# Kernel optimization log

Measured on AMD Instinct MI355X. Metric: run time of the kernel, lower is better.

## Reference

```python
import jax, jax.numpy as jnp
import numpy as np

NUM_HEADS = 8
NUM_LAYER = 4


def setup_inputs() -> dict:
    key = jax.random.key(0)
    k1, k2, k3, k4, k5, k6, k7 = jax.random.split(key, 7)
    bs, num, C = 2, 2048, 256
    H0 = (jax.random.uniform(k1, (bs, num, num)) < 0.3).astype(jnp.float32)
    vertex_feat = jax.random.normal(k2, (bs, C, num), dtype=jnp.float32)
    edge_feat = jax.random.normal(k3, (bs, C, num), dtype=jnp.float32)
    s = 1.0 / np.sqrt(C)
    # Conv1d(kernel_size=1) weights, squeezed to [C_out, C_in]
    Wq = jax.random.uniform(k4, (C, C), minval=-s, maxval=s, dtype=jnp.float32)
    bq = jax.random.uniform(k5, (C,), minval=-s, maxval=s, dtype=jnp.float32)
    Wk = jax.random.uniform(k6, (C, C), minval=-s, maxval=s, dtype=jnp.float32)
    bk = jax.random.uniform(k7, (C,), minval=-s, maxval=s, dtype=jnp.float32)
    return {"H0": H0, "vertex_feat": vertex_feat, "edge_feat": edge_feat,
            "Wq": Wq, "bq": bq, "Wk": Wk, "bk": bk, "iter": 1}


def reference(H0, vertex_feat, edge_feat, Wq, bq, Wk, bk, iter):
    bs, num, _ = H0.shape
    C = vertex_feat.shape[1]
    h = NUM_HEADS
    d = C // h
    # 1x1 Conv1d == per-position linear; reshape to heads: [bs, h, d, num]
    Q = (jnp.einsum('oc,bcn->bon', Wq, vertex_feat) + bq[None, :, None]).reshape(bs, h, d, num)
    K = (jnp.einsum('oc,bcn->bon', Wk, edge_feat) + bk[None, :, None]).reshape(bs, h, d, num)
    attn = jnp.einsum('bhco,bhci->bhoi', Q, K) / np.sqrt(d)  # [bs, h, num, num]
    # attention_mask = (1 - H0).masked_fill((1-H0).bool(), -1e9)
    m = 1.0 - H0
    m = jnp.where(m != 0, jnp.float32(-1e9), m)
    score = jax.nn.sigmoid(attn + m[:, None, :, :]).sum(axis=1) / h  # [bs, num, num]
    # top-k row thresholding (k static: iter is a python int)
    k = max(1, round(num * 0.1 * (NUM_LAYER - 1 - iter)))
    topk_vals = jax.lax.top_k(score, k)[0]           # sorted descending
    a_min = topk_vals[..., -1:]                      # row-wise k-th largest
    W = jnp.where(score >= a_min, score, jnp.float32(0.0))
    H = jnp.where(W > 0, H0, jnp.float32(0.0))
    # degree normalizations (1e-10 keeps them finite; torch isinf branch is a no-op)
    De_n_1 = (1.0 / (H.sum(axis=1) + 1e-10))[..., None]  # [bs, num, 1]
    Dv_n_1 = (1.0 / (H.sum(axis=2) + 1e-10))[..., None]  # [bs, num, 1]
    # F.normalize(W.sum(dim=1), dim=1): L2 normalize with eps=1e-12
    W_edge = W.sum(axis=1)
    W_edge = W_edge / jnp.maximum(jnp.linalg.norm(W_edge, axis=1, keepdims=True), 1e-12)
    W_edge = W_edge[..., None]  # [bs, num, 1]
    return (H, W, De_n_1, Dv_n_1, W_edge)
```

## Files before the change

kernel.cpp:

```cpp
#include <hip/hip_runtime.h>
#include <math.h>

#define NUM 2048
#define CDIM 256
#define NUM_LAYER 4

typedef short bf16x8 __attribute__((ext_vector_type(8)));
typedef unsigned short u16x8 __attribute__((ext_vector_type(8)));
typedef float f32x4 __attribute__((ext_vector_type(4)));

static __device__ __forceinline__ unsigned short f2bf(float f) {
  unsigned u = __float_as_uint(f);
  unsigned r = 0x7FFFu + ((u >> 16) & 1u);
  return (unsigned short)((u + r) >> 16);
}
static __device__ __forceinline__ float bf2f(unsigned short h) {
  return __uint_as_float(((unsigned)h) << 16);
}

__global__ __launch_bounds__(256) void proj_kernel(
    const float* __restrict__ Wq, const float* __restrict__ bq,
    const float* __restrict__ Wk, const float* __restrict__ bk,
    const float* __restrict__ vf, const float* __restrict__ ef,
    unsigned short* __restrict__ Qhi, unsigned short* __restrict__ Qmd,
    unsigned short* __restrict__ Qlo, unsigned short* __restrict__ Khi,
    unsigned short* __restrict__ Kmd, unsigned short* __restrict__ Klo)
{
  const int z = blockIdx.z;
  const int b = z >> 1, mm2 = z & 1;
  const float* __restrict__ Wmat = mm2 ? Wk : Wq;
  const float* __restrict__ bias = mm2 ? bk : bq;
  const float* __restrict__ x = (mm2 ? ef : vf) + (size_t)b * CDIM * NUM;
  unsigned short* __restrict__ ohi = mm2 ? Khi : Qhi;
  unsigned short* __restrict__ omd = mm2 ? Kmd : Qmd;
  unsigned short* __restrict__ olo = mm2 ? Klo : Qlo;

  const int n0 = blockIdx.x * 64;
  const int o0 = blockIdx.y * 64;
  __shared__ float Xs[32][65];
  __shared__ float Ws[64][33];
  __shared__ float T[64][69];
  const int t = threadIdx.x;
  const int tx = t & 15, ty = t >> 4;

  float acc[4][4];
  #pragma unroll
  for (int a = 0; a < 4; a++)
    #pragma unroll
    for (int c = 0; c < 4; c++) acc[a][c] = 0.0f;

  for (int cc = 0; cc < CDIM; cc += 32) {
    #pragma unroll
    for (int e = 0; e < 2; e++) {
      int f = t * 2 + e;
      int row = f >> 4, c4 = f & 15;
      const float4 v = *(const float4*)(&x[(size_t)(cc + row) * NUM + n0 + c4 * 4]);
      Xs[row][c4*4+0] = v.x; Xs[row][c4*4+1] = v.y;
      Xs[row][c4*4+2] = v.z; Xs[row][c4*4+3] = v.w;
    }
    #pragma unroll
    for (int e = 0; e < 2; e++) {
      int f = t * 2 + e;
      int row = f >> 3, c4 = f & 7;
      const float4 v = *(const float4*)(&Wmat[(size_t)(o0 + row) * CDIM + cc + c4 * 4]);
      Ws[row][c4*4+0] = v.x; Ws[row][c4*4+1] = v.y;
      Ws[row][c4*4+2] = v.z; Ws[row][c4*4+3] = v.w;
    }
    __syncthreads();
    #pragma unroll
    for (int kk = 0; kk < 32; kk++) {
      float xv[4], wv[4];
      #pragma unroll
      for (int j = 0; j < 4; j++) xv[j] = Xs[kk][tx*4+j];
      #pragma unroll
      for (int j = 0; j < 4; j++) wv[j] = Ws[ty*4+j][kk];
      #pragma unroll
      for (int oi = 0; oi < 4; oi++)
        #pragma unroll
        for (int ni = 0; ni < 4; ni++)
          acc[oi][ni] = fmaf(wv[oi], xv[ni], acc[oi][ni]);
    }
    __syncthreads();
  }
  float bb[4];
  #pragma unroll
  for (int oi = 0; oi < 4; oi++) bb[oi] = bias[o0 + ty*4 + oi];
  #pragma unroll
  for (int ni = 0; ni < 4; ni++)
    #pragma unroll
    for (int oi = 0; oi < 4; oi++)
      T[tx*4+ni][ty*4+oi] = acc[oi][ni] + bb[oi];
  __syncthreads();
  const int n_l = t >> 2;
  const int oc  = (t & 3) * 16;
  float xv[16];
  #pragma unroll
  for (int j = 0; j < 16; j++) xv[j] = T[n_l][oc + j];
  unsigned short hi[16], md[16], lo[16];
  #pragma unroll
  for (int j = 0; j < 16; j++) {
    unsigned short h = f2bf(xv[j]);
    float r1 = xv[j] - bf2f(h);
    unsigned short mdj = f2bf(r1);
    float r2 = r1 - bf2f(mdj);
    hi[j] = h; md[j] = mdj; lo[j] = f2bf(r2);
  }
  const size_t gb = ((size_t)b * NUM + n0 + n_l) * CDIM + o0 + oc;
  *(u16x8*)&ohi[gb]   = *(u16x8*)&hi[0];
  *(u16x8*)&ohi[gb+8] = *(u16x8*)&hi[8];
  *(u16x8*)&omd[gb]   = *(u16x8*)&md[0];
  *(u16x8*)&omd[gb+8] = *(u16x8*)&md[8];
  *(u16x8*)&olo[gb]   = *(u16x8*)&lo[0];
  *(u16x8*)&olo[gb+8] = *(u16x8*)&lo[8];
}

__global__ __launch_bounds__(256) void score_kernel(
    const unsigned short* __restrict__ Qhi, const unsigned short* __restrict__ Qmd,
    const unsigned short* __restrict__ Qlo, const unsigned short* __restrict__ Khi,
    const unsigned short* __restrict__ Kmd, const unsigned short* __restrict__ Klo,
    const float* __restrict__ H0, float* __restrict__ score)
{
  const int b = blockIdx.z;
  const int i0 = blockIdx.x * 128;
  const int o0 = blockIdx.y * 128;
  const int t = threadIdx.x, lane = t & 63, wave = t >> 6;
  const int m = lane & 15, quad = lane >> 4;
  const int obl = (wave >> 1) * 64;
  const int ibl = (wave & 1) * 64;

  __shared__ unsigned short qsh[3][128][36];
  __shared__ unsigned short ksh[3][128][36];

  const int srow = t >> 2;
  const int schk = (t & 3) * 8;

  f32x4 ssum[4][4];
  #pragma unroll
  for (int a = 0; a < 4; a++)
    #pragma unroll
    for (int c = 0; c < 4; c++) ssum[a][c] = (f32x4){0.f, 0.f, 0.f, 0.f};

  const float SC = -1.4426950408889634f * 0.17677669529663687f;

  u16x8 pq[3][2], pk[3][2];
  #pragma unroll
  for (int e = 0; e < 2; e++) {
    const size_t go = ((size_t)b * NUM + o0 + srow + 64*e) * CDIM + schk;
    const size_t gi = ((size_t)b * NUM + i0 + srow + 64*e) * CDIM + schk;
    pq[0][e] = *(const u16x8*)&Qhi[go];
    pq[1][e] = *(const u16x8*)&Qmd[go];
    pq[2][e] = *(const u16x8*)&Qlo[go];
    pk[0][e] = *(const u16x8*)&Khi[gi];
    pk[1][e] = *(const u16x8*)&Kmd[gi];
    pk[2][e] = *(const u16x8*)&Klo[gi];
  }

  for (int h = 0; h < 8; h++) {
    __syncthreads();
    #pragma unroll
    for (int e = 0; e < 2; e++) {
      #pragma unroll
      for (int cp = 0; cp < 3; cp++) {
        *(u16x8*)&qsh[cp][srow + 64*e][schk] = pq[cp][e];
        *(u16x8*)&ksh[cp][srow + 64*e][schk] = pk[cp][e];
      }
    }
    __syncthreads();
    if (h < 7) {
      const int coff = (h + 1) * 32 + schk;
      #pragma unroll
      for (int e = 0; e < 2; e++) {
        const size_t go = ((size_t)b * NUM + o0 + srow + 64*e) * CDIM + coff;
        const size_t gi = ((size_t)b * NUM + i0 + srow + 64*e) * CDIM + coff;
        pq[0][e] = *(const u16x8*)&Qhi[go];
        pq[1][e] = *(const u16x8*)&Qmd[go];
        pq[2][e] = *(const u16x8*)&Qlo[go];
        pk[0][e] = *(const u16x8*)&Khi[gi];
        pk[1][e] = *(const u16x8*)&Kmd[gi];
        pk[2][e] = *(const u16x8*)&Klo[gi];
      }
    }
    bf16x8 a[4][3];
    #pragma unroll
    for (int ot = 0; ot < 4; ot++)
      #pragma unroll
      for (int cp = 0; cp < 3; cp++)
        a[ot][cp] = *(const bf16x8*)&qsh[cp][obl + ot*16 + m][quad*8];
    #pragma unroll
    for (int it = 0; it < 4; it++) {
      const bf16x8 b0 = *(const bf16x8*)&ksh[0][ibl + it*16 + m][quad*8];
      const bf16x8 b1 = *(const bf16x8*)&ksh[1][ibl + it*16 + m][quad*8];
      const bf16x8 b2 = *(const bf16x8*)&ksh[2][ibl + it*16 + m][quad*8];
      #pragma unroll
      for (int ot = 0; ot < 4; ot++) {
        f32x4 c = (f32x4){0.f, 0.f, 0.f, 0.f};
        c = __builtin_amdgcn_mfma_f32_16x16x32_bf16(a[ot][0], b0, c, 0, 0, 0);
        c = __builtin_amdgcn_mfma_f32_16x16x32_bf16(a[ot][0], b1, c, 0, 0, 0);
        c = __builtin_amdgcn_mfma_f32_16x16x32_bf16(a[ot][1], b0, c, 0, 0, 0);
        c = __builtin_amdgcn_mfma_f32_16x16x32_bf16(a[ot][1], b1, c, 0, 0, 0);
        c = __builtin_amdgcn_mfma_f32_16x16x32_bf16(a[ot][0], b2, c, 0, 0, 0);
        c = __builtin_amdgcn_mfma_f32_16x16x32_bf16(a[ot][2], b0, c, 0, 0, 0);
        #pragma unroll
        for (int r = 0; r < 4; r++)
          ssum[ot][it][r] += __builtin_amdgcn_rcpf(1.0f + __builtin_amdgcn_exp2f(c[r] * SC));
      }
    }
  }
  const int ob = o0 + obl, ib = i0 + ibl;
  #pragma unroll
  for (int ot = 0; ot < 4; ot++)
    #pragma unroll
    for (int it = 0; it < 4; it++)
      #pragma unroll
      for (int r = 0; r < 4; r++) {
        const int row = ob + ot*16 + quad*4 + r;
        const int col = ib + it*16 + m;
        const size_t idx = ((size_t)b * NUM + row) * NUM + col;
        score[idx] = H0[idx] * ssum[ot][it][r] * 0.125f;
      }
}

__global__ __launch_bounds__(256) void topk_apply_kernel(
    float* __restrict__ scoreW, float* __restrict__ Hout,
    const int* __restrict__ iterp, float* __restrict__ DvOut)
{
  const int row = blockIdx.x;
  __shared__ unsigned int hist[4][256];
  __shared__ unsigned int cum[257];
  __shared__ unsigned int s_sel, s_rem;
  __shared__ float red[4];
  const int t = threadIdx.x;
  const int wid = t >> 6, lane = t & 63;
  unsigned int* __restrict__ srow = (unsigned int*)scoreW + (size_t)row * NUM;

  const uint4 va = ((const uint4*)srow)[t*2];
  const uint4 vb = ((const uint4*)srow)[t*2+1];
  unsigned int v[8] = {va.x, va.y, va.z, va.w, vb.x, vb.y, vb.z, vb.w};

  const int it = iterp[0];
  int k = (int)((double)NUM * 0.1 * (double)(NUM_LAYER - 1 - it) + 0.5);
  if (k < 1) k = 1;
  if (k > NUM) k = NUM;

  unsigned int prefix = 0;
  unsigned int rem = (unsigned int)k;
  unsigned int* hflat = &hist[0][0];

  for (int pass = 3; pass >= 0; pass--) {
    const int shift = pass * 8;
    const unsigned int pmask = (pass == 3) ? 0u : (0xFFFFFFFFu << (shift + 8));
    #pragma unroll
    for (int j = 0; j < 4; j++) hflat[t + 256*j] = 0;
    __syncthreads();
    unsigned int zc = 0;
    #pragma unroll
    for (int j = 0; j < 8; j++) {
      unsigned int val = v[j];
      if ((val & pmask) == prefix) {
        unsigned int bin = (val >> shift) & 255u;
        if (bin) atomicAdd(&hist[wid][bin], 1u);
        else zc++;
      }
    }
    #pragma unroll
    for (int off = 32; off > 0; off >>= 1) zc += __shfl_down(zc, off, 64);
    if (lane == 0 && zc) atomicAdd(&hist[wid][0], zc);
    __syncthreads();
    if (t < 64) {
      unsigned int T[4], s[4];
      #pragma unroll
      for (int q = 0; q < 4; q++)
        T[q] = hist[0][t*4+q] + hist[1][t*4+q] + hist[2][t*4+q] + hist[3][t*4+q];
      s[3] = T[3];
      s[2] = T[2] + s[3];
      s[1] = T[1] + s[2];
      s[0] = T[0] + s[1];
      unsigned int tot = s[0];
      #pragma unroll
      for (int off = 1; off < 64; off <<= 1) {
        unsigned int y = __shfl_down(tot, off, 64);
        if (lane + off < 64) tot += y;
      }
      const unsigned int above_chunk = tot - s[0];
      #pragma unroll
      for (int q = 0; q < 4; q++) cum[t*4+q] = s[q] + above_chunk;
      if (t == 0) cum[256] = 0;
    }
    __syncthreads();
    unsigned int c = cum[t], above = cum[t + 1];
    if (c >= rem && above < rem) { s_sel = (unsigned int)t; s_rem = rem - above; }
    __syncthreads();
    prefix |= (s_sel << shift);
    rem = s_rem;
    __syncthreads();
  }

  const unsigned int amin = prefix;
  float* __restrict__ Hrow = Hout + (size_t)row * NUM;
  unsigned int w[8];
  float hh[8];
  float cnt = 0.0f;
  #pragma unroll
  for (int j = 0; j < 8; j++) {
    w[j] = (v[j] >= amin) ? v[j] : 0u;
    hh[j] = (w[j] != 0u) ? 1.0f : 0.0f;
    cnt += hh[j];
  }
  ((uint4*)srow)[t*2]   = make_uint4(w[0], w[1], w[2], w[3]);
  ((uint4*)srow)[t*2+1] = make_uint4(w[4], w[5], w[6], w[7]);
  ((float4*)Hrow)[t*2]   = make_float4(hh[0], hh[1], hh[2], hh[3]);
  ((float4*)Hrow)[t*2+1] = make_float4(hh[4], hh[5], hh[6], hh[7]);
  #pragma unroll
  for (int off = 32; off > 0; off >>= 1) cnt += __shfl_down(cnt, off, 64);
  if (lane == 0) red[wid] = cnt;
  __syncthreads();
  if (t == 0) {
    float tot = red[0] + red[1] + red[2] + red[3];
    DvOut[row] = 1.0f / (tot + 1e-10f);
  }
}

__global__ __launch_bounds__(256) void colsum_kernel(
    const float* __restrict__ Wmat,
    float* __restrict__ colH, float* __restrict__ colW)
{
  const int b = blockIdx.z;
  const int i = blockIdx.x * 256 + threadIdx.x;
  const int o0 = blockIdx.y * 128;
  float sh = 0.0f, sw = 0.0f;
  for (int o = 0; o < 128; o++) {
    size_t idx = ((size_t)b * NUM + o0 + o) * NUM + i;
    float w = Wmat[idx];
    sw += w;
    sh += (w > 0.0f) ? 1.0f : 0.0f;
  }
  atomicAdd(&colH[b * NUM + i], sh);
  atomicAdd(&colW[b * NUM + i], sw);
}

__global__ __launch_bounds__(1024) void finalize_kernel(
    const float* __restrict__ colH, const float* __restrict__ colW,
    float* __restrict__ De, float* __restrict__ We)
{
  const int b = blockIdx.x;
  const int t = threadIdx.x;
  float cw[2];
  float sq = 0.0f;
  #pragma unroll
  for (int j = 0; j < 2; j++) {
    int i = t + 1024*j;
    float ch = colH[b * NUM + i];
    De[b * NUM + i] = 1.0f / (ch + 1e-10f);
    cw[j] = colW[b * NUM + i];
    sq += cw[j] * cw[j];
  }
  for (int off = 32; off > 0; off >>= 1) sq += __shfl_down(sq, off, 64);
  __shared__ float red[16];
  __shared__ float s_nrm;
  if ((t & 63) == 0) red[t >> 6] = sq;
  __syncthreads();
  if (t == 0) {
    float tot = 0.0f;
    for (int i2 = 0; i2 < 16; i2++) tot += red[i2];
    s_nrm = fmaxf(sqrtf(tot), 1e-12f);
  }
  __syncthreads();
  #pragma unroll
  for (int j = 0; j < 2; j++)
    We[b * NUM + t + 1024*j] = cw[j] / s_nrm;
}

extern "C" void kernel_launch(void* const* d_in, const int* in_sizes, int n_in,
                              void* d_out, int out_size, void* d_ws, size_t ws_size,
                              hipStream_t stream) {
  const float* H0 = (const float*)d_in[0];
  const float* vf = (const float*)d_in[1];
  const float* ef = (const float*)d_in[2];
  const float* Wq = (const float*)d_in[3];
  const float* bq = (const float*)d_in[4];
  const float* Wk = (const float*)d_in[5];
  const float* bk = (const float*)d_in[6];
  const int* iter = (const int*)d_in[7];

  float* out = (float*)d_out;
  const size_t nH = (size_t)2 * NUM * NUM;
  float* Hout  = out;
  float* Wout  = out + nH;
  float* DeOut = out + 2 * nH;
  float* DvOut = DeOut + 2 * NUM;
  float* WeOut = DvOut + 2 * NUM;

  float* colH = (float*)d_ws;
  float* colW = colH + 2 * NUM;

  const size_t nC = (size_t)2 * NUM * CDIM;
  unsigned short* base = (unsigned short*)Hout;
  unsigned short* Qhi = base;
  unsigned short* Qmd = base + nC;
  unsigned short* Qlo = base + 2 * nC;
  unsigned short* Khi = base + 3 * nC;
  unsigned short* Kmd = base + 4 * nC;
  unsigned short* Klo = base + 5 * nC;

  hipMemsetAsync(d_ws, 0, (size_t)2 * 2 * NUM * sizeof(float), stream);

  proj_kernel<<<dim3(NUM/64, CDIM/64, 4), 256, 0, stream>>>(
      Wq, bq, Wk, bk, vf, ef, Qhi, Qmd, Qlo, Khi, Kmd, Klo);
  score_kernel<<<dim3(NUM/128, NUM/128, 2), 256, 0, stream>>>(
      Qhi, Qmd, Qlo, Khi, Kmd, Klo, H0, Wout);
  topk_apply_kernel<<<dim3(2 * NUM), 256, 0, stream>>>(Wout, Hout, iter, DvOut);
  colsum_kernel<<<dim3(NUM/256, NUM/128, 2), 256, 0, stream>>>(Wout, colH, colW);
  finalize_kernel<<<dim3(2), 1024, 0, stream>>>(colH, colW, DeOut, WeOut);
}
```

Before: 206.4 us.

## Shrink score tile to 128x64 and move H0 masking into topk kernel

The score kernel now uses 128-thread blocks over a 128x64 output tile, which doubles the block count and shrinks the LDS tile with tighter padding. The H0 load and multiply move from the score epilogue into the top-k kernel, which reads H0 alongside the score row. The H output is now written in the column-sum kernel instead of the top-k kernel. The goal is better occupancy and load balance in the score GEMM and fewer scattered epilogue loads, at the cost of more K-side reloads, since each Q tile is reused across fewer columns.

```diff
diff --git a/kernel.cpp b/kernel.cpp
--- a/kernel.cpp
+++ b/kernel.cpp
@@ -114,25 +114,21 @@
   *(u16x8*)&olo[gb+8] = *(u16x8*)&lo[8];
 }
 
-__global__ __launch_bounds__(256) void score_kernel(
+__global__ __launch_bounds__(128) void score_kernel(
     const unsigned short* __restrict__ Qhi, const unsigned short* __restrict__ Qmd,
     const unsigned short* __restrict__ Qlo, const unsigned short* __restrict__ Khi,
     const unsigned short* __restrict__ Kmd, const unsigned short* __restrict__ Klo,
-    const float* __restrict__ H0, float* __restrict__ score)
+    float* __restrict__ score)
 {
   const int b = blockIdx.z;
-  const int i0 = blockIdx.x * 128;
+  const int i0 = blockIdx.x * 64;
   const int o0 = blockIdx.y * 128;
   const int t = threadIdx.x, lane = t & 63, wave = t >> 6;
   const int m = lane & 15, quad = lane >> 4;
-  const int obl = (wave >> 1) * 64;
-  const int ibl = (wave & 1) * 64;
-
-  __shared__ unsigned short qsh[3][128][36];
-  __shared__ unsigned short ksh[3][128][36];
-
-  const int srow = t >> 2;
-  const int schk = (t & 3) * 8;
+  const int obl = wave * 64;
+
+  __shared__ unsigned short qsh[3][128][34];
+  __shared__ unsigned short ksh[3][64][34];
 
   f32x4 ssum[4][4];
   #pragma unroll
@@ -142,14 +138,19 @@
 
   const float SC = -1.4426950408889634f * 0.17677669529663687f;
 
-  u16x8 pq[3][2], pk[3][2];
-  #pragma unroll
-  for (int e = 0; e < 2; e++) {
-    const size_t go = ((size_t)b * NUM + o0 + srow + 64*e) * CDIM + schk;
-    const size_t gi = ((size_t)b * NUM + i0 + srow + 64*e) * CDIM + schk;
+  u16x8 pq[3][4], pk[3][2];
+  #pragma unroll
+  for (int e = 0; e < 4; e++) {
+    const int f = t + 128 * e, row = f >> 2, ch = (f & 3) * 8;
+    const size_t go = ((size_t)b * NUM + o0 + row) * CDIM + ch;
     pq[0][e] = *(const u16x8*)&Qhi[go];
     pq[1][e] = *(const u16x8*)&Qmd[go];
     pq[2][e] = *(const u16x8*)&Qlo[go];
+  }
+  #pragma unroll
+  for (int e = 0; e < 2; e++) {
+    const int f = t + 128 * e, row = f >> 2, ch = (f & 3) * 8;
+    const size_t gi = ((size_t)b * NUM + i0 + row) * CDIM + ch;
     pk[0][e] = *(const u16x8*)&Khi[gi];
     pk[1][e] = *(const u16x8*)&Kmd[gi];
     pk[2][e] = *(const u16x8*)&Klo[gi];
@@ -158,23 +159,34 @@
   for (int h = 0; h < 8; h++) {
     __syncthreads();
     #pragma unroll
+    for (int e = 0; e < 4; e++) {
+      const int f = t + 128 * e, row = f >> 2, ch = (f & 3) * 8;
+      #pragma unroll
+      for (int cp = 0; cp < 3; cp++)
+        *(u16x8*)&qsh[cp][row][ch] = pq[cp][e];
+    }
+    #pragma unroll
     for (int e = 0; e < 2; e++) {
-      #pragma unroll
-      for (int cp = 0; cp < 3; cp++) {
-        *(u16x8*)&qsh[cp][srow + 64*e][schk] = pq[cp][e];
-        *(u16x8*)&ksh[cp][srow + 64*e][schk] = pk[cp][e];
-      }
+      const int f = t + 128 * e, row = f >> 2, ch = (f & 3) * 8;
+      #pragma unroll
+      for (int cp = 0; cp < 3; cp++)
+        *(u16x8*)&ksh[cp][row][ch] = pk[cp][e];
     }
     __syncthreads();
     if (h < 7) {
-      const int coff = (h + 1) * 32 + schk;
-      #pragma unroll
-      for (int e = 0; e < 2; e++) {
-        const size_t go = ((size_t)b * NUM + o0 + srow + 64*e) * CDIM + coff;
-        const size_t gi = ((size_t)b * NUM + i0 + srow + 64*e) * CDIM + coff;
+      const int coff = (h + 1) * 32;
+      #pragma unroll
+      for (int e = 0; e < 4; e++) {
+        const int f = t + 128 * e, row = f >> 2, ch = (f & 3) * 8;
+        const size_t go = ((size_t)b * NUM + o0 + row) * CDIM + coff + ch;
         pq[0][e] = *(const u16x8*)&Qhi[go];
         pq[1][e] = *(const u16x8*)&Qmd[go];
         pq[2][e] = *(const u16x8*)&Qlo[go];
+      }
+      #pragma unroll
+      for (int e = 0; e < 2; e++) {
+        const int f = t + 128 * e, row = f >> 2, ch = (f & 3) * 8;
+        const size_t gi = ((size_t)b * NUM + i0 + row) * CDIM + coff + ch;
         pk[0][e] = *(const u16x8*)&Khi[gi];
         pk[1][e] = *(const u16x8*)&Kmd[gi];
         pk[2][e] = *(const u16x8*)&Klo[gi];
@@ -188,9 +200,9 @@
         a[ot][cp] = *(const bf16x8*)&qsh[cp][obl + ot*16 + m][quad*8];
     #pragma unroll
     for (int it = 0; it < 4; it++) {
-      const bf16x8 b0 = *(const bf16x8*)&ksh[0][ibl + it*16 + m][quad*8];
-      const bf16x8 b1 = *(const bf16x8*)&ksh[1][ibl + it*16 + m][quad*8];
-      const bf16x8 b2 = *(const bf16x8*)&ksh[2][ibl + it*16 + m][quad*8];
+      const bf16x8 b0 = *(const bf16x8*)&ksh[0][it*16 + m][quad*8];
+      const bf16x8 b1 = *(const bf16x8*)&ksh[1][it*16 + m][quad*8];
+      const bf16x8 b2 = *(const bf16x8*)&ksh[2][it*16 + m][quad*8];
       #pragma unroll
       for (int ot = 0; ot < 4; ot++) {
         f32x4 c = (f32x4){0.f, 0.f, 0.f, 0.f};
@@ -206,7 +218,7 @@
       }
     }
   }
-  const int ob = o0 + obl, ib = i0 + ibl;
+  const int ob = o0 + obl;
   #pragma unroll
   for (int ot = 0; ot < 4; ot++)
     #pragma unroll
@@ -214,14 +226,13 @@
       #pragma unroll
       for (int r = 0; r < 4; r++) {
         const int row = ob + ot*16 + quad*4 + r;
-        const int col = ib + it*16 + m;
-        const size_t idx = ((size_t)b * NUM + row) * NUM + col;
-        score[idx] = H0[idx] * ssum[ot][it][r] * 0.125f;
+        const int col = i0 + it*16 + m;
+        score[((size_t)b * NUM + row) * NUM + col] = ssum[ot][it][r] * 0.125f;
       }
 }
 
 __global__ __launch_bounds__(256) void topk_apply_kernel(
-    float* __restrict__ scoreW, float* __restrict__ Hout,
+    float* __restrict__ scoreW, const float* __restrict__ H0,
     const int* __restrict__ iterp, float* __restrict__ DvOut)
 {
   const int row = blockIdx.x;
@@ -232,10 +243,21 @@
   const int t = threadIdx.x;
   const int wid = t >> 6, lane = t & 63;
   unsigned int* __restrict__ srow = (unsigned int*)scoreW + (size_t)row * NUM;
-
-  const uint4 va = ((const uint4*)srow)[t*2];
-  const uint4 vb = ((const uint4*)srow)[t*2+1];
-  unsigned int v[8] = {va.x, va.y, va.z, va.w, vb.x, vb.y, vb.z, vb.w};
+  const float* __restrict__ h0row = H0 + (size_t)row * NUM;
+
+  const uint4 sa = ((const uint4*)srow)[t*2];
+  const uint4 sb = ((const uint4*)srow)[t*2+1];
+  const float4 ha = ((const float4*)h0row)[t*2];
+  const float4 hb = ((const float4*)h0row)[t*2+1];
+  unsigned int v[8];
+  v[0] = __float_as_uint(ha.x * __uint_as_float(sa.x));
+  v[1] = __float_as_uint(ha.y * __uint_as_float(sa.y));
+  v[2] = __float_as_uint(ha.z * __uint_as_float(sa.z));
+  v[3] = __float_as_uint(ha.w * __uint_as_float(sa.w));
+  v[4] = __float_as_uint(hb.x * __uint_as_float(sb.x));
+  v[5] = __float_as_uint(hb.y * __uint_as_float(sb.y));
+  v[6] = __float_as_uint(hb.z * __uint_as_float(sb.z));
+  v[7] = __float_as_uint(hb.w * __uint_as_float(sb.w));
 
   const int it = iterp[0];
   int k = (int)((double)NUM * 0.1 * (double)(NUM_LAYER - 1 - it) + 0.5);
@@ -296,20 +318,15 @@
   }
 
   const unsigned int amin = prefix;
-  float* __restrict__ Hrow = Hout + (size_t)row * NUM;
   unsigned int w[8];
-  float hh[8];
   float cnt = 0.0f;
   #pragma unroll
   for (int j = 0; j < 8; j++) {
     w[j] = (v[j] >= amin) ? v[j] : 0u;
-    hh[j] = (w[j] != 0u) ? 1.0f : 0.0f;
-    cnt += hh[j];
+    cnt += (w[j] != 0u) ? 1.0f : 0.0f;
   }
   ((uint4*)srow)[t*2]   = make_uint4(w[0], w[1], w[2], w[3]);
   ((uint4*)srow)[t*2+1] = make_uint4(w[4], w[5], w[6], w[7]);
-  ((float4*)Hrow)[t*2]   = make_float4(hh[0], hh[1], hh[2], hh[3]);
-  ((float4*)Hrow)[t*2+1] = make_float4(hh[4], hh[5], hh[6], hh[7]);
   #pragma unroll
   for (int off = 32; off > 0; off >>= 1) cnt += __shfl_down(cnt, off, 64);
   if (lane == 0) red[wid] = cnt;
@@ -321,7 +338,7 @@
 }
 
 __global__ __launch_bounds__(256) void colsum_kernel(
-    const float* __restrict__ Wmat,
+    const float* __restrict__ Wmat, float* __restrict__ Hout,
     float* __restrict__ colH, float* __restrict__ colW)
 {
   const int b = blockIdx.z;
@@ -331,8 +348,10 @@
   for (int o = 0; o < 128; o++) {
     size_t idx = ((size_t)b * NUM + o0 + o) * NUM + i;
     float w = Wmat[idx];
+    float hh = (w > 0.0f) ? 1.0f : 0.0f;
+    Hout[idx] = hh;
     sw += w;
-    sh += (w > 0.0f) ? 1.0f : 0.0f;
+    sh += hh;
   }
   atomicAdd(&colH[b * NUM + i], sh);
   atomicAdd(&colW[b * NUM + i], sw);
@@ -406,9 +425,9 @@
 
   proj_kernel<<<dim3(NUM/64, CDIM/64, 4), 256, 0, stream>>>(
       Wq, bq, Wk, bk, vf, ef, Qhi, Qmd, Qlo, Khi, Kmd, Klo);
-  score_kernel<<<dim3(NUM/128, NUM/128, 2), 256, 0, stream>>>(
-      Qhi, Qmd, Qlo, Khi, Kmd, Klo, H0, Wout);
-  topk_apply_kernel<<<dim3(2 * NUM), 256, 0, stream>>>(Wout, Hout, iter, DvOut);
-  colsum_kernel<<<dim3(NUM/256, NUM/128, 2), 256, 0, stream>>>(Wout, colH, colW);
+  score_kernel<<<dim3(NUM/64, NUM/128, 2), 128, 0, stream>>>(
+      Qhi, Qmd, Qlo, Khi, Kmd, Klo, Wout);
+  topk_apply_kernel<<<dim3(2 * NUM), 256, 0, stream>>>(Wout, H0, iter, DvOut);
+  colsum_kernel<<<dim3(NUM/256, NUM/128, 2), 256, 0, stream>>>(Wout, Hout, colH, colW);
   finalize_kernel<<<dim3(2), 1024, 0, stream>>>(colH, colW, DeOut, WeOut);
 }
```

Result: slower. 211.1 us (+2.3%).
